# Performance work log

Measured on AMD Instinct MI355X. Metric: run time of the kernel, lower is better.

Reference implementation:

```python
import jax, jax.numpy as jnp
import numpy as np

N, E, G = 50000, 1600000, 64
N_SPECIES, D_ATTR, D, N_RBF = 16, 16, 32, 8
CUTOFF = 5.0
SCALE, SHIFT = 1.0, 0.0


def setup_inputs() -> dict:
    key = jax.random.key(0)
    ks = jax.random.split(key, 20)

    def w(k, shape):
        fan_in = shape[-2] if len(shape) > 1 else shape[-1]
        return jax.random.normal(k, shape, dtype=jnp.float32) / np.sqrt(fan_in)

    return {
        "x": jax.random.randint(ks[0], (N, 1), 0, N_SPECIES),
        "pos": 3.0 * jax.random.normal(ks[1], (N, 3), dtype=jnp.float32),
        "edge_index": jax.random.randint(ks[2], (2, E), 0, N),
        "period_vec": 0.1 * jax.random.normal(ks[3], (E, 3), dtype=jnp.float32),
        "batch": jnp.sort(jax.random.randint(ks[4], (N,), 0, G)),
        "W_elem": w(ks[5], (N_SPECIES, D_ATTR)),
        "W0": w(ks[6], (D_ATTR, D)),
        "b0": jnp.zeros((D,), jnp.float32),
        "Wr1": w(ks[7], (3, N_RBF, D)),
        "br1": jnp.zeros((3, D), jnp.float32),
        "Wr2": w(ks[8], (3, D, D)),
        "Wmsg": w(ks[9], (3, D, D)),
        "Wattr": w(ks[10], (3, D_ATTR, D)),
        "Wself": w(ks[11], (3, D, D)),
        "bconv": jnp.zeros((3, D), jnp.float32),
        "wsh": w(ks[12], (3, 4)),
        "Wp1": w(ks[13], (D, 16)),
        "bp1": jnp.zeros((16,), jnp.float32),
        "Wp2": w(ks[14], (16, 1)),
        "bp2": jnp.zeros((1,), jnp.float32),
    }


def reference(x, pos, edge_index, period_vec, batch, W_elem, W0, b0, Wr1, br1,
              Wr2, Wmsg, Wattr, Wself, bconv, wsh, Wp1, bp1, Wp2, bp2):
    src, dst = edge_index[0], edge_index[1]

    # node_attr_layer: species embedding (gather), then first_atom_embed linear
    x_attr = W_elem[x[:, 0]]                              # [N, D_ATTR]
    h = x_attr @ W0 + b0                                  # [N, D]

    # edge_attr_layer: PBC edge vectors, lengths, l<=1 spherical harmonics
    edge_vec = pos[dst] - pos[src] + period_vec           # [E, 3]
    edge_len = jnp.linalg.norm(edge_vec, axis=-1, keepdims=True)  # [E, 1]
    unit = edge_vec / (edge_len + 1e-9)
    edge_sh = jnp.concatenate([jnp.ones_like(edge_len), unit], axis=-1)  # [E, 4]

    # edge_embedding_layer: Gaussian radial basis of edge lengths
    centers = jnp.linspace(0.0, CUTOFF, N_RBF, dtype=pos.dtype)
    gamma = jnp.asarray((N_RBF / CUTOFF) ** 2, pos.dtype)
    rbf = jnp.exp(-gamma * (edge_len - centers) ** 2)     # [E, N_RBF]

    # 3 conv layers: gather -> per-edge transform -> scatter-sum -> node update
    for i in range(3):
        rw = jax.nn.relu(rbf @ Wr1[i] + br1[i]) @ Wr2[i]  # [E, D] radial MLP
        sh_w = edge_sh @ wsh[i]                           # [E] sh mixing
        msg = (h[src] @ Wmsg[i]) * rw * sh_w[:, None]     # [E, D]
        agg = jax.ops.segment_sum(msg, dst, num_segments=N)  # [N, D]
        h = jax.nn.silu(agg + x_attr @ Wattr[i] + h @ Wself[i] + bconv[i])

    # post_conv layers
    h = jax.nn.silu(h @ Wp1 + bp1)                        # [N, 16]
    h = (h @ Wp2 + bp2)[:, 0]                             # [N] (squeeze)

    # scatter-sum pooling over graphs + affine energy scaling
    e = jax.ops.segment_sum(h, batch, num_segments=G)     # [G]
    return (e * SCALE + SHIFT)[:, None]                   # [G, 1]
```

## Files before the change

kernel.cpp:

```cpp
#include <hip/hip_runtime.h>
#include <hip/hip_fp16.h>
#include <math.h>

constexpr int N_NODES  = 50000;
constexpr int N_EDGES  = 1600000;
constexpr int G_GRAPHS = 64;
constexpr int D        = 32;
constexpr int D_ATTR   = 16;
constexpr int N_RBF    = 8;

constexpr int   TBL      = 8192;
constexpr int   TBL_ROWS = TBL + 1;
constexpr float LMAX     = 10.0f;

constexpr int BUCKET = 80;

constexpr int NT     = 64;
constexpr int NTILES = (N_NODES + NT - 1) / NT;
constexpr int TCAP   = 2432;
constexpr int EPB    = 4096;
constexpr int NBLK1  = (N_EDGES + EPB - 1) / EPB;

constexpr int NSLOT = NTILES * NT * BUCKET;

typedef unsigned int  uint4v  __attribute__((ext_vector_type(4)));
typedef unsigned int  uint2v  __attribute__((ext_vector_type(2)));

__device__ __forceinline__ float silu(float x) {
    return x / (1.0f + __expf(-x));
}
__device__ __forceinline__ float h2f_bits(unsigned short u) {
    return __half2float(__ushort_as_half(u));
}

__global__ void node_init_kernel(const int* __restrict__ x,
                                 const float* __restrict__ W_elem,
                                 const float* __restrict__ W0,
                                 const float* __restrict__ b0,
                                 const float* __restrict__ Wmsg0,
                                 const float* __restrict__ Wself0,
                                 const float* __restrict__ Wattr,
                                 const float* __restrict__ bconv,
                                 __half* __restrict__ hm0,
                                 float* __restrict__ hs0,
                                 float* __restrict__ xa1,
                                 float* __restrict__ xa2,
                                 int* __restrict__ tile_cursor,
                                 float* __restrict__ out) {
    int t = blockIdx.x * blockDim.x + threadIdx.x;
    if (t < NTILES) tile_cursor[t] = 0;
    if (t < G_GRAPHS) out[t] = 0.0f;
    int n = t >> 5, c = t & 31;
    if (n >= N_NODES) return;
    int sp = x[n];
    const float* we = W_elem + sp * D_ATTR;
    float xv = (c < D_ATTR) ? we[c] : 0.0f;
    float acc = b0[c];
#pragma unroll
    for (int a = 0; a < D_ATTR; ++a) acc += we[a] * W0[a * D + c];
    float m = 0.0f, s = 0.0f;
#pragma unroll
    for (int j = 0; j < D; ++j) {
        float hj = __shfl(acc, j, 32);
        m = fmaf(hj, Wmsg0[j * D + c], m);
        s = fmaf(hj, Wself0[j * D + c], s);
    }
    float a0 = bconv[0 * D + c], a1 = bconv[1 * D + c], a2 = bconv[2 * D + c];
#pragma unroll
    for (int j = 0; j < D_ATTR; ++j) {
        float xj = __shfl(xv, j, 32);
        a0 = fmaf(xj, Wattr[0 * D_ATTR * D + j * D + c], a0);
        a1 = fmaf(xj, Wattr[1 * D_ATTR * D + j * D + c], a1);
        a2 = fmaf(xj, Wattr[2 * D_ATTR * D + j * D + c], a2);
    }
    hm0[n * D + c] = __float2half(m);
    hs0[n * D + c] = s + a0;
    xa1[n * D + c] = a1;
    xa2[n * D + c] = a2;
}

__global__ __launch_bounds__(256) void scatter_kernel(const int* __restrict__ eidx,
                                                      const float* __restrict__ pos,
                                                      const float* __restrict__ period,
                                                      const float* __restrict__ wsh,
                                                      int* __restrict__ tile_cursor,
                                                      uint4v* __restrict__ bins) {
    __shared__ int hist[NTILES];
    __shared__ int basev[NTILES];
    int tid = threadIdx.x;
    int e0 = blockIdx.x * EPB;
    for (int i = tid; i < NTILES; i += 256) hist[i] = 0;
    __syncthreads();
#pragma unroll 4
    for (int i = 0; i < EPB / 256; ++i) {
        int e = e0 + tid + 256 * i;
        if (e < N_EDGES) atomicAdd(&hist[eidx[N_EDGES + e] >> 6], 1);
    }
    __syncthreads();
    for (int t = tid; t < NTILES; t += 256) {
        int cnt = hist[t];
        basev[t] = (cnt > 0) ? atomicAdd(&tile_cursor[t], cnt) : 0;
        hist[t] = 0;
    }
    __syncthreads();
    for (int i = 0; i < EPB / 256; ++i) {
        int e = e0 + tid + 256 * i;
        if (e >= N_EDGES) continue;
        int s = eidx[e];
        int d = eidx[N_EDGES + e];
        float vx = pos[d * 3 + 0] - pos[s * 3 + 0] + period[e * 3 + 0];
        float vy = pos[d * 3 + 1] - pos[s * 3 + 1] + period[e * 3 + 1];
        float vz = pos[d * 3 + 2] - pos[s * 3 + 2] + period[e * 3 + 2];
        float len = sqrtf(vx * vx + vy * vy + vz * vz);
        float inv = 1.0f / (len + 1e-9f);
        int idx = (int)fminf(len * ((float)TBL / LMAX) + 0.5f, (float)TBL);
        float sw[3];
#pragma unroll
        for (int l = 0; l < 3; ++l)
            sw[l] = wsh[l * 4 + 0] + (vx * wsh[l * 4 + 1] + vy * wsh[l * 4 + 2] + vz * wsh[l * 4 + 3]) * inv;
        int tile = d >> 6;
        int rank = atomicAdd(&hist[tile], 1);
        int slot = basev[tile] + rank;
        if (slot < TCAP) {
            unsigned u0 = (unsigned)__half_as_ushort(__float2half(sw[0]));
            unsigned u1 = (unsigned)__half_as_ushort(__float2half(sw[1]));
            unsigned u2 = (unsigned)__half_as_ushort(__float2half(sw[2]));
            uint4v r;
            r.x = (unsigned)s | ((unsigned)idx << 16);
            r.y = (unsigned)(d & (NT - 1));
            r.z = u0 | (u1 << 16);
            r.w = u2;
            bins[(size_t)tile * TCAP + slot] = r;
        }
    }
}

__global__ __launch_bounds__(256) void shuffle_kernel(const uint4v* __restrict__ bins,
                                                      const int* __restrict__ tile_cursor,
                                                      unsigned int* __restrict__ xs,
                                                      unsigned short* __restrict__ swp,
                                                      int* __restrict__ count) {
    __shared__ int lcur[NT];
    int tile = blockIdx.x;
    int tid = threadIdx.x;
    if (tid < NT) lcur[tid] = 0;
    __syncthreads();
    int cnt = tile_cursor[tile];
    if (cnt > TCAP) cnt = TCAP;
    const uint4v* base = bins + (size_t)tile * TCAP;
    for (int i = tid; i < cnt; i += 256) {
        uint4v r = __builtin_nontemporal_load(base + i);
        int dl = (int)(r.y & 63u);
        int slot = atomicAdd(&lcur[dl], 1);
        if (slot < BUCKET) {
            size_t g = (size_t)(tile * NT + dl) * BUCKET + slot;
            xs[g] = r.x;
            swp[0 * (size_t)NSLOT + g] = (unsigned short)(r.z & 0xFFFFu);
            swp[1 * (size_t)NSLOT + g] = (unsigned short)(r.z >> 16);
            swp[2 * (size_t)NSLOT + g] = (unsigned short)(r.w & 0xFFFFu);
        }
    }
    __syncthreads();
    if (tid < NT) {
        int node = tile * NT + tid;
        if (node < N_NODES) {
            int c = lcur[tid];
            count[node] = c < BUCKET ? c : BUCKET;
        }
    }
}

__global__ void table_kernel(const float* __restrict__ Wr1,
                             const float* __restrict__ br1,
                             const float* __restrict__ Wr2,
                             __half* __restrict__ table) {
    int t = blockIdx.x * blockDim.x + threadIdx.x;
    if (t >= 3 * TBL_ROWS) return;
    int l = t / TBL_ROWS;
    int idx = t % TBL_ROWS;
    float len = (float)idx * (LMAX / (float)TBL);
    const float gamma = (8.0f / 5.0f) * (8.0f / 5.0f);
    float rbf[N_RBF];
#pragma unroll
    for (int k = 0; k < N_RBF; ++k) {
        float dd = len - (float)k * (5.0f / 7.0f);
        rbf[k] = __expf(-gamma * dd * dd);
    }
    float out[D];
#pragma unroll
    for (int c = 0; c < D; ++c) out[c] = 0.0f;
    for (int j = 0; j < D; ++j) {
        float z = br1[l * D + j];
#pragma unroll
        for (int k = 0; k < N_RBF; ++k) z += rbf[k] * Wr1[l * N_RBF * D + k * D + j];
        z = fmaxf(z, 0.0f);
        const float* w2 = Wr2 + l * D * D + j * D;
#pragma unroll
        for (int c = 0; c < D; ++c) out[c] += z * w2[c];
    }
    __half* dst = table + ((size_t)(l * TBL_ROWS + idx)) * D;
#pragma unroll
    for (int c = 0; c < D; ++c) dst[c] = __float2half(out[c]);
}

template <int LAYER, bool NEXT>
__global__ void conv_kernel(const __half* __restrict__ hm,
                            const float* __restrict__ hs,
                            const unsigned int* __restrict__ xs,
                            const unsigned short* __restrict__ swp,
                            const int* __restrict__ count,
                            const __half* __restrict__ table,
                            const float* __restrict__ Wmsg_next,
                            const float* __restrict__ Wself_next,
                            const float* __restrict__ xa_next,
                            __half* __restrict__ hm_out,
                            float* __restrict__ hs_out,
                            float* __restrict__ h_final) {
    int gtid = blockIdx.x * blockDim.x + threadIdx.x;
    int node = gtid >> 6;
    if (node >= N_NODES) return;
    int lane = threadIdx.x & 63;
    int qw = lane >> 4;
    int q  = lane & 15;

    const __half2* tab2 = (const __half2*)(table + ((size_t)LAYER * TBL_ROWS) * D);
    const __half2* hm2  = (const __half2*)hm;
    const unsigned short* swb = swp + (size_t)LAYER * NSLOT;
    int cnt = count[node];
    int beg = node * BUCKET;
    int end = beg + cnt;

    float ax = 0.0f, ay = 0.0f;
    for (int base = beg; base < end; base += 32) {
        int o0 = base + qw * 4;
        int o1 = o0 + 16;
        uint4v x0 = __builtin_nontemporal_load((const uint4v*)(xs + o0));
        uint4v x1 = __builtin_nontemporal_load((const uint4v*)(xs + o1));
        uint2v w0 = __builtin_nontemporal_load((const uint2v*)(swb + o0));
        uint2v w1 = __builtin_nontemporal_load((const uint2v*)(swb + o1));
        unsigned u[8];
        unsigned short wv[8];
        u[0] = x0.x; u[1] = x0.y; u[2] = x0.z; u[3] = x0.w;
        u[4] = x1.x; u[5] = x1.y; u[6] = x1.z; u[7] = x1.w;
        wv[0] = (unsigned short)(w0.x & 0xFFFFu); wv[1] = (unsigned short)(w0.x >> 16);
        wv[2] = (unsigned short)(w0.y & 0xFFFFu); wv[3] = (unsigned short)(w0.y >> 16);
        wv[4] = (unsigned short)(w1.x & 0xFFFFu); wv[5] = (unsigned short)(w1.x >> 16);
        wv[6] = (unsigned short)(w1.y & 0xFFFFu); wv[7] = (unsigned short)(w1.y >> 16);
#pragma unroll
        for (int j = 0; j < 8; ++j) {
            int slot = (j < 4) ? (o0 + j) : (o1 + j - 4);
            bool valid = slot < end;
            unsigned uu = valid ? u[j] : 0u;
            float sw = valid ? h2f_bits(wv[j]) : 0.0f;
            int s = (int)(uu & 0xFFFFu);
            int i = (int)(uu >> 16);
            float2 tf = __half22float2(tab2[i * 16 + q]);
            float2 mf = __half22float2(hm2[s * 16 + q]);
            ax = fmaf(tf.x * mf.x, sw, ax);
            ay = fmaf(tf.y * mf.y, sw, ay);
        }
    }
    ax += __shfl_xor(ax, 16);
    ax += __shfl_xor(ax, 32);
    ay += __shfl_xor(ay, 16);
    ay += __shfl_xor(ay, 32);

    int c = lane & 31;
    float vx = __shfl(ax, c >> 1);
    float vy = __shfl(ay, c >> 1);
    float agg = (c & 1) ? vy : vx;

    if ((lane >> 5) == 0) {
        float hn = silu(agg + hs[node * D + c]);
        if (NEXT) {
            float m = 0.0f, s2 = 0.0f;
#pragma unroll
            for (int j = 0; j < D; ++j) {
                float hj = __shfl(hn, j);
                m  = fmaf(hj, Wmsg_next[j * D + c], m);
                s2 = fmaf(hj, Wself_next[j * D + c], s2);
            }
            hm_out[node * D + c] = __float2half(m);
            hs_out[node * D + c] = s2 + xa_next[node * D + c];
        } else {
            h_final[node * D + c] = hn;
        }
    }
}

__global__ void readout_kernel(const float* __restrict__ h,
                               const int* __restrict__ batch,
                               const float* __restrict__ Wp1,
                               const float* __restrict__ bp1,
                               const float* __restrict__ Wp2,
                               const float* __restrict__ bp2,
                               float* __restrict__ out) {
    int n = blockIdx.x * blockDim.x + threadIdx.x;
    float s = 0.0f;
    int b = -1;
    if (n < N_NODES) {
        b = batch[n];
        const float* hrow = h + n * D;
        float acc2 = bp2[0];
#pragma unroll
        for (int m = 0; m < 16; ++m) {
            float a = bp1[m];
#pragma unroll
            for (int j = 0; j < D; ++j) a += hrow[j] * Wp1[j * 16 + m];
            acc2 += silu(a) * Wp2[m];
        }
        s = acc2;
    }
    unsigned long long valid = __ballot(n < N_NODES);
    if (valid == 0ull) return;
    int firstLane = __ffsll(valid) - 1;
    int b0v = __shfl(b, firstLane);
    bool ok = (b == b0v) || (n >= N_NODES);
    if (__all(ok)) {
#pragma unroll
        for (int o = 32; o > 0; o >>= 1) s += __shfl_down(s, o);
        if ((threadIdx.x & 63) == 0) atomicAdd(out + b0v, s);
    } else {
        if (n < N_NODES) atomicAdd(out + b, s);
    }
}

extern "C" void kernel_launch(void* const* d_in, const int* in_sizes, int n_in,
                              void* d_out, int out_size, void* d_ws, size_t ws_size,
                              hipStream_t stream) {
    const int*   x      = (const int*)d_in[0];
    const float* pos    = (const float*)d_in[1];
    const int*   eidx   = (const int*)d_in[2];
    const float* period = (const float*)d_in[3];
    const int*   batch  = (const int*)d_in[4];
    const float* W_elem = (const float*)d_in[5];
    const float* W0     = (const float*)d_in[6];
    const float* b0     = (const float*)d_in[7];
    const float* Wr1    = (const float*)d_in[8];
    const float* br1    = (const float*)d_in[9];
    const float* Wr2    = (const float*)d_in[10];
    const float* Wmsg   = (const float*)d_in[11];
    const float* Wattr  = (const float*)d_in[12];
    const float* Wself  = (const float*)d_in[13];
    const float* bconv  = (const float*)d_in[14];
    const float* wsh    = (const float*)d_in[15];
    const float* Wp1    = (const float*)d_in[16];
    const float* bp1    = (const float*)d_in[17];
    const float* Wp2    = (const float*)d_in[18];
    const float* bp2    = (const float*)d_in[19];

    char* base = (char*)d_ws;
    size_t off = 0;
    auto carve = [&](size_t bytes) -> void* {
        void* p = base + off;
        off = (off + bytes + 255) & ~(size_t)255;
        return p;
    };
    __half*         hm_a        = (__half*)carve((size_t)N_NODES * D * 2);
    __half*         hm_b        = (__half*)carve((size_t)N_NODES * D * 2);
    float*          hs_a        = (float*)carve((size_t)N_NODES * D * 4);
    float*          hs_b        = (float*)carve((size_t)N_NODES * D * 4);
    float*          xa1         = (float*)carve((size_t)N_NODES * D * 4);
    float*          xa2         = (float*)carve((size_t)N_NODES * D * 4);
    float*          h_final     = (float*)carve((size_t)N_NODES * D * 4);
    unsigned int*   xs          = (unsigned int*)carve((size_t)NSLOT * 4);
    unsigned short* swp         = (unsigned short*)carve((size_t)3 * NSLOT * 2);
    uint4v*         bins        = (uint4v*)carve((size_t)NTILES * TCAP * 16);
    int*            tile_cursor = (int*)carve((size_t)NTILES * 4);
    int*            count       = (int*)carve((size_t)NTILES * NT * 4);
    __half*         table       = (__half*)carve((size_t)3 * TBL_ROWS * D * 2);
    (void)ws_size; (void)in_sizes; (void)n_in; (void)out_size;

    node_init_kernel<<<(N_NODES * 32 + 255) / 256, 256, 0, stream>>>(
        x, W_elem, W0, b0, Wmsg + 0 * D * D, Wself + 0 * D * D, Wattr, bconv,
        hm_a, hs_a, xa1, xa2, tile_cursor, (float*)d_out);
    scatter_kernel<<<NBLK1, 256, 0, stream>>>(eidx, pos, period, wsh, tile_cursor, bins);
    table_kernel<<<(3 * TBL_ROWS + 127) / 128, 128, 0, stream>>>(Wr1, br1, Wr2, table);
    shuffle_kernel<<<NTILES, 256, 0, stream>>>(bins, tile_cursor, xs, swp, count);

    int cgrid = (N_NODES * 64 + 255) / 256;
    conv_kernel<0, true><<<cgrid, 256, 0, stream>>>(
        hm_a, hs_a, xs, swp, count, table, Wmsg + 1 * D * D, Wself + 1 * D * D, xa1,
        hm_b, hs_b, nullptr);
    conv_kernel<1, true><<<cgrid, 256, 0, stream>>>(
        hm_b, hs_b, xs, swp, count, table, Wmsg + 2 * D * D, Wself + 2 * D * D, xa2,
        hm_a, hs_a, nullptr);
    conv_kernel<2, false><<<cgrid, 256, 0, stream>>>(
        hm_a, hs_a, xs, swp, count, table, nullptr, nullptr, nullptr,
        nullptr, nullptr, h_final);

    readout_kernel<<<(N_NODES + 255) / 256, 256, 0, stream>>>(h_final, batch, Wp1, bp1, Wp2, bp2,
                                                              (float*)d_out);
}
```

Before: 404.1 us.

## Replace block-local histogram binning with direct per-edge global atomics

```diff
diff --git a/kernel.cpp b/kernel.cpp
--- a/kernel.cpp
+++ b/kernel.cpp
@@ -18,8 +18,9 @@
 constexpr int NT     = 64;
 constexpr int NTILES = (N_NODES + NT - 1) / NT;
 constexpr int TCAP   = 2432;
-constexpr int EPB    = 4096;
-constexpr int NBLK1  = (N_EDGES + EPB - 1) / EPB;
+
+constexpr int SBLK  = 256;
+constexpr int NBLK1 = (N_EDGES + SBLK - 1) / SBLK;
 
 constexpr int NSLOT = NTILES * NT * BUCKET;
 
@@ -79,63 +80,43 @@
     xa2[n * D + c] = a2;
 }
 
-__global__ __launch_bounds__(256) void scatter_kernel(const int* __restrict__ eidx,
-                                                      const float* __restrict__ pos,
-                                                      const float* __restrict__ period,
-                                                      const float* __restrict__ wsh,
-                                                      int* __restrict__ tile_cursor,
-                                                      uint4v* __restrict__ bins) {
-    __shared__ int hist[NTILES];
-    __shared__ int basev[NTILES];
-    int tid = threadIdx.x;
-    int e0 = blockIdx.x * EPB;
-    for (int i = tid; i < NTILES; i += 256) hist[i] = 0;
-    __syncthreads();
-#pragma unroll 4
-    for (int i = 0; i < EPB / 256; ++i) {
-        int e = e0 + tid + 256 * i;
-        if (e < N_EDGES) atomicAdd(&hist[eidx[N_EDGES + e] >> 6], 1);
-    }
-    __syncthreads();
-    for (int t = tid; t < NTILES; t += 256) {
-        int cnt = hist[t];
-        basev[t] = (cnt > 0) ? atomicAdd(&tile_cursor[t], cnt) : 0;
-        hist[t] = 0;
-    }
-    __syncthreads();
-    for (int i = 0; i < EPB / 256; ++i) {
-        int e = e0 + tid + 256 * i;
-        if (e >= N_EDGES) continue;
-        int s = eidx[e];
-        int d = eidx[N_EDGES + e];
-        float vx = pos[d * 3 + 0] - pos[s * 3 + 0] + period[e * 3 + 0];
-        float vy = pos[d * 3 + 1] - pos[s * 3 + 1] + period[e * 3 + 1];
-        float vz = pos[d * 3 + 2] - pos[s * 3 + 2] + period[e * 3 + 2];
-        float len = sqrtf(vx * vx + vy * vy + vz * vz);
-        float inv = 1.0f / (len + 1e-9f);
-        int idx = (int)fminf(len * ((float)TBL / LMAX) + 0.5f, (float)TBL);
-        float sw[3];
-#pragma unroll
-        for (int l = 0; l < 3; ++l)
-            sw[l] = wsh[l * 4 + 0] + (vx * wsh[l * 4 + 1] + vy * wsh[l * 4 + 2] + vz * wsh[l * 4 + 3]) * inv;
-        int tile = d >> 6;
-        int rank = atomicAdd(&hist[tile], 1);
-        int slot = basev[tile] + rank;
-        if (slot < TCAP) {
-            unsigned u0 = (unsigned)__half_as_ushort(__float2half(sw[0]));
-            unsigned u1 = (unsigned)__half_as_ushort(__float2half(sw[1]));
-            unsigned u2 = (unsigned)__half_as_ushort(__float2half(sw[2]));
-            uint4v r;
-            r.x = (unsigned)s | ((unsigned)idx << 16);
-            r.y = (unsigned)(d & (NT - 1));
-            r.z = u0 | (u1 << 16);
-            r.w = u2;
-            bins[(size_t)tile * TCAP + slot] = r;
-        }
-    }
-}
-
-__global__ __launch_bounds__(256) void shuffle_kernel(const uint4v* __restrict__ bins,
+__global__ __launch_bounds__(SBLK) void scatter_kernel(const int* __restrict__ eidx,
+                                                       const float* __restrict__ pos,
+                                                       const float* __restrict__ period,
+                                                       const float* __restrict__ wsh,
+                                                       int* __restrict__ tile_cursor,
+                                                       uint4v* __restrict__ bins) {
+    int e = blockIdx.x * SBLK + threadIdx.x;
+    if (e >= N_EDGES) return;
+    int s = eidx[e];
+    int d = eidx[N_EDGES + e];
+    float vx = pos[d * 3 + 0] - pos[s * 3 + 0] + period[e * 3 + 0];
+    float vy = pos[d * 3 + 1] - pos[s * 3 + 1] + period[e * 3 + 1];
+    float vz = pos[d * 3 + 2] - pos[s * 3 + 2] + period[e * 3 + 2];
+    float len = sqrtf(vx * vx + vy * vy + vz * vz);
+    float inv = 1.0f / (len + 1e-9f);
+    int idx = (int)fminf(len * ((float)TBL / LMAX) + 0.5f, (float)TBL);
+    float sw[3];
+#pragma unroll
+    for (int l = 0; l < 3; ++l)
+        sw[l] = wsh[l * 4 + 0] +
+                (vx * wsh[l * 4 + 1] + vy * wsh[l * 4 + 2] + vz * wsh[l * 4 + 3]) * inv;
+    int tile = d >> 6;
+    int slot = atomicAdd(&tile_cursor[tile], 1);
+    if (slot < TCAP) {
+        unsigned u0 = (unsigned)__half_as_ushort(__float2half(sw[0]));
+        unsigned u1 = (unsigned)__half_as_ushort(__float2half(sw[1]));
+        unsigned u2 = (unsigned)__half_as_ushort(__float2half(sw[2]));
+        uint4v r;
+        r.x = (unsigned)s | ((unsigned)idx << 16);
+        r.y = (unsigned)(d & (NT - 1));
+        r.z = u0 | (u1 << 16);
+        r.w = u2;
+        bins[(size_t)tile * TCAP + slot] = r;
+    }
+}
+
+__global__ __launch_bounds__(512) void shuffle_kernel(const uint4v* __restrict__ bins,
                                                       const int* __restrict__ tile_cursor,
                                                       unsigned int* __restrict__ xs,
                                                       unsigned short* __restrict__ swp,
@@ -148,7 +129,7 @@
     int cnt = tile_cursor[tile];
     if (cnt > TCAP) cnt = TCAP;
     const uint4v* base = bins + (size_t)tile * TCAP;
-    for (int i = tid; i < cnt; i += 256) {
+    for (int i = tid; i < cnt; i += 512) {
         uint4v r = __builtin_nontemporal_load(base + i);
         int dl = (int)(r.y & 63u);
         int slot = atomicAdd(&lcur[dl], 1);
@@ -374,9 +355,9 @@
     node_init_kernel<<<(N_NODES * 32 + 255) / 256, 256, 0, stream>>>(
         x, W_elem, W0, b0, Wmsg + 0 * D * D, Wself + 0 * D * D, Wattr, bconv,
         hm_a, hs_a, xa1, xa2, tile_cursor, (float*)d_out);
-    scatter_kernel<<<NBLK1, 256, 0, stream>>>(eidx, pos, period, wsh, tile_cursor, bins);
+    scatter_kernel<<<NBLK1, SBLK, 0, stream>>>(eidx, pos, period, wsh, tile_cursor, bins);
     table_kernel<<<(3 * TBL_ROWS + 127) / 128, 128, 0, stream>>>(Wr1, br1, Wr2, table);
-    shuffle_kernel<<<NTILES, 256, 0, stream>>>(bins, tile_cursor, xs, swp, count);
+    shuffle_kernel<<<NTILES, 512, 0, stream>>>(bins, tile_cursor, xs, swp, count);
 
     int cgrid = (N_NODES * 64 + 255) / 256;
     conv_kernel<0, true><<<cgrid, 256, 0, stream>>>(
```

New measurement: 733.5 us. +81.5%, slower.
